# Optimization experiments

Hardware: AMD Instinct MI355X
Metric: run time of the kernel (lower is better)

The kernel has to match this reference:

```python
import jax, jax.numpy as jnp
import numpy as np

EMBED_DIM = 1024
NUM_HEADS = 16
HEAD_DIM = EMBED_DIM // NUM_HEADS


def setup_inputs() -> dict:
    key = jax.random.key(0)
    ks = jax.random.split(key, 9)
    B, S, D = 4, 2048, EMBED_DIM
    s = 1.0 / np.sqrt(D)
    inp = {
        "x": jax.random.normal(ks[0], (B, S, D), dtype=jnp.float32),
        "Wq": jax.random.uniform(ks[1], (D, D), jnp.float32, -s, s),
        "bq": jax.random.uniform(ks[2], (D,), jnp.float32, -s, s),
        "Wk": jax.random.uniform(ks[3], (D, D), jnp.float32, -s, s),
        "bk": jax.random.uniform(ks[4], (D,), jnp.float32, -s, s),
        "Wv": jax.random.uniform(ks[5], (D, D), jnp.float32, -s, s),
        "bv": jax.random.uniform(ks[6], (D,), jnp.float32, -s, s),
        "Wo": jax.random.uniform(ks[7], (D, D), jnp.float32, -s, s),
        "bo": jax.random.uniform(ks[8], (D,), jnp.float32, -s, s),
    }
    return inp


def reference(x, Wq, bq, Wk, bk, Wv, bv, Wo, bo):
    B, S, D = x.shape
    H, Hd = NUM_HEADS, HEAD_DIM
    scale = 1.0 / jnp.sqrt(jnp.asarray(Hd, x.dtype))

    def split_heads(t):  # (B,S,D) -> (B,H,S,Hd)
        return t.reshape(B, S, H, Hd).transpose(0, 2, 1, 3)

    q = split_heads(x @ Wq + bq)
    k = split_heads(x @ Wk + bk)
    v = split_heads(x @ Wv + bv)

    scores = jnp.einsum("bhqd,bhkd->bhqk", q, k) * scale
    attn = jax.nn.softmax(scores, axis=-1)  # dropout is identity in eval mode
    out = jnp.einsum("bhqk,bhkd->bhqd", attn, v)
    out = out.transpose(0, 2, 1, 3).reshape(B, S, D)
    return out @ Wo + bo
```

## Files before the change

### kernel.cpp

```cpp
#include <hip/hip_runtime.h>
#include <cstdint>

typedef unsigned short u16;
typedef uint32_t u32;
typedef float f32x4 __attribute__((ext_vector_type(4)));
typedef short s16x8 __attribute__((ext_vector_type(8)));
typedef u16 u16x4 __attribute__((ext_vector_type(4)));
typedef u32 u32x2 __attribute__((ext_vector_type(2)));
typedef u32 u32x4 __attribute__((ext_vector_type(4)));

__device__ __forceinline__ u16 f2bf(float f) {
  u32 u = __builtin_bit_cast(u32, f);
  u += 0x7FFFu + ((u >> 16) & 1u);
  return (u16)(u >> 16);
}

__device__ __forceinline__ u32 pack2bf_trunc(float lo, float hi) {
  return __builtin_amdgcn_perm(__builtin_bit_cast(u32, hi),
                               __builtin_bit_cast(u32, lo), 0x07060302u);
}

template <typename T>
__device__ __forceinline__ T ldv(const void* p) {
  T v;
  __builtin_memcpy(&v, __builtin_assume_aligned(p, 16), sizeof(T));
  return v;
}

__device__ __forceinline__ void gload_lds16(const void* g, void* l) {
  __builtin_amdgcn_global_load_lds((const __attribute__((address_space(1))) void*)g,
                                   (__attribute__((address_space(3))) void*)l, 16, 0, 0);
}

__global__ __launch_bounds__(256) void cvt_x_k(const float* __restrict__ in,
                                               u16* __restrict__ out) {
  const int i = (blockIdx.x * 256 + threadIdx.x) * 4;
  float4 v = *(const float4*)(in + i);
  u16x4 o;
  o.x = f2bf(v.x); o.y = f2bf(v.y); o.z = f2bf(v.z); o.w = f2bf(v.w);
  *(u16x4*)(out + i) = o;
}

__global__ __launch_bounds__(256) void prep_w_k(const float* __restrict__ Wq,
                                                const float* __restrict__ Wk,
                                                const float* __restrict__ Wv,
                                                const float* __restrict__ Wo,
                                                u16* __restrict__ out) {
  __shared__ u16 t[64][72];
  const float* W = (blockIdx.z == 0) ? Wq : (blockIdx.z == 1) ? Wk
                  : (blockIdx.z == 2) ? Wv : Wo;
  u16* O = out + (size_t)blockIdx.z * 1024 * 1024;
  const int n0 = blockIdx.x * 64, k0 = blockIdx.y * 64;
  const int tid = threadIdx.x;
#pragma unroll
  for (int i = 0; i < 16; ++i) {
    int e = i * 256 + tid;
    int r = e >> 6, c = e & 63;
    t[r][c] = f2bf(W[(size_t)(k0 + r) * 1024 + n0 + c]);
  }
  __syncthreads();
#pragma unroll
  for (int i = 0; i < 16; ++i) {
    int e = i * 256 + tid;
    int rr = e >> 6, cc = e & 63;
    O[(size_t)(n0 + rr) * 1024 + k0 + cc] = t[cc][rr];
  }
}

__global__ __launch_bounds__(256) void gemm_qkv_k(const u16* __restrict__ A,
                                                  const u16* __restrict__ Wt,
                                                  const float* __restrict__ bq,
                                                  const float* __restrict__ bk,
                                                  const float* __restrict__ bv,
                                                  u16* __restrict__ Qh,
                                                  u16* __restrict__ Kh,
                                                  u16* __restrict__ Vt,
                                                  float qscale) {
  constexpr int K = 1024;
  __shared__ __attribute__((aligned(16))) u16 As[2][128][64];
  __shared__ __attribute__((aligned(16))) u16 Bs[2][128][64];
  const int tid = threadIdx.x;
  const int l = tid & 63, w = tid >> 6;
  const int lr = l & 15, lg = l >> 4;
  const int m0 = blockIdx.x * 128;
  const int ng = blockIdx.y * 128;
  const int seg = ng >> 10;
  const int n0 = ng & 1023;
  const u16* Bt = Wt + ((size_t)seg << 20);
  const int wr = (w >> 1) * 64, wc = (w & 1) * 64;
  const int rA = tid >> 3;
  const int cA = (tid & 7) * 8;

  f32x4 acc[4][4] = {};

#define GSTAGE(buf, kt)                                                         \
  do {                                                                          \
    _Pragma("unroll")                                                           \
    for (int i = 0; i < 4; ++i) {                                               \
      gload_lds16(A + (size_t)(m0 + i * 32 + rA) * K + (kt) + cA,               \
                  &As[buf][0][0] + (size_t)(i * 256 + w * 64) * 8);             \
      gload_lds16(Bt + (size_t)(n0 + i * 32 + rA) * K + (kt) + cA,              \
                  &Bs[buf][0][0] + (size_t)(i * 256 + w * 64) * 8);             \
    }                                                                           \
  } while (0)

  GSTAGE(0, 0);
  for (int ki = 0; ki < 16; ++ki) {
    const int cur = ki & 1;
    if (ki < 15) {
      GSTAGE(cur ^ 1, (ki + 1) * 64);
      asm volatile("s_waitcnt vmcnt(8)" ::: "memory");
    } else {
      asm volatile("s_waitcnt vmcnt(0)" ::: "memory");
    }
    __builtin_amdgcn_sched_barrier(0);
    __builtin_amdgcn_s_barrier();
    __builtin_amdgcn_sched_barrier(0);
#pragma unroll
    for (int kk = 0; kk < 2; ++kk) {
      s16x8 a[4], b[4];
#pragma unroll
      for (int mi = 0; mi < 4; ++mi)
        a[mi] = ldv<s16x8>(&As[cur][wr + mi * 16 + lr][kk * 32 + lg * 8]);
#pragma unroll
      for (int ni = 0; ni < 4; ++ni)
        b[ni] = ldv<s16x8>(&Bs[cur][wc + ni * 16 + lr][kk * 32 + lg * 8]);
#pragma unroll
      for (int mi = 0; mi < 4; ++mi)
#pragma unroll
        for (int ni = 0; ni < 4; ++ni)
          acc[mi][ni] = __builtin_amdgcn_mfma_f32_16x16x32_bf16(a[mi], b[ni], acc[mi][ni], 0, 0, 0);
    }
    __builtin_amdgcn_sched_barrier(0);
    __builtin_amdgcn_s_barrier();
  }
#undef GSTAGE

  const float* bias = (seg == 0) ? bq : (seg == 1) ? bk : bv;
  const float scale = (seg == 0) ? qscale : 1.0f;
  u16* outp = (seg == 0) ? Qh : (seg == 1) ? Kh : Vt;

  u16* Cb = &As[0][0][0];
  const int bb = m0 >> 11;
  const int sbase = m0 & 2047;

#pragma unroll
  for (int p = 0; p < 2; ++p) {
    __syncthreads();
    if ((wc >> 6) == p) {
#pragma unroll
      for (int ni = 0; ni < 4; ++ni) {
        const int c = ni * 16 + lr;
        const float bvv = bias[n0 + p * 64 + c];
#pragma unroll
        for (int mi = 0; mi < 4; ++mi) {
#pragma unroll
          for (int r = 0; r < 4; ++r) {
            const int row = wr + mi * 16 + lg * 4 + r;
            Cb[row * 64 + ((((c >> 3) ^ (row & 7)) << 3) | (c & 7))] =
                f2bf((acc[mi][ni][r] + bvv) * scale);
          }
        }
      }
    }
    __syncthreads();
    const int h = (n0 + p * 64) >> 6;
    if (seg <= 1) {
      const int row = tid >> 1;
      const int s = sbase + row;
#pragma unroll
      for (int j = 0; j < 4; ++j) {
        const int c = (tid & 1) * 32 + j * 8;
        s16x8 v = ldv<s16x8>(&Cb[row * 64 + (((c >> 3) ^ (row & 7)) << 3)]);
        const int chunk = (seg == 0) ? (c >> 3) : (((c >> 3) ^ (s & 7)) & 7);
        *(s16x8*)(outp + ((size_t)((bb << 4) + h) * 2048 + s) * 64 + (chunk << 3)) = v;
      }
    } else {
      const int hd = tid & 63;
#pragma unroll
      for (int j = 0; j < 4; ++j) {
        const int s0 = ((tid >> 6) * 4 + j) * 8;
        u16 vals[8];
#pragma unroll
        for (int i = 0; i < 8; ++i) {
          const int row = s0 + i;
          vals[i] = Cb[row * 64 + ((((hd >> 3) ^ (row & 7)) << 3) | (hd & 7))];
        }
        const int sl = sbase + s0;
        const int swz = (((sl >> 3) & 7) ^ (hd & 7)) & 7;
        *(s16x8*)(outp + ((size_t)((bb << 4) + h) * 64 + hd) * 2048 +
                  ((sl & ~63) | (swz << 3))) = *(s16x8*)vals;
      }
    }
  }
}

__global__ __launch_bounds__(256) void gemm_o_k(const u16* __restrict__ A,
                                                const u16* __restrict__ Bt,
                                                const float* __restrict__ bias,
                                                float* __restrict__ outp) {
  constexpr int K = 1024;
  __shared__ __attribute__((aligned(16))) u16 As[2][128][64];
  __shared__ __attribute__((aligned(16))) u16 Bs[2][128][64];
  const int tid = threadIdx.x;
  const int l = tid & 63, w = tid >> 6;
  const int lr = l & 15, lg = l >> 4;
  const int m0 = blockIdx.x * 128, n0 = blockIdx.y * 128;
  const int wr = (w >> 1) * 64, wc = (w & 1) * 64;
  const int rA = tid >> 3;
  const int cA = (tid & 7) * 8;

  f32x4 acc[4][4] = {};

#define GSTAGE(buf, kt)                                                         \
  do {                                                                          \
    _Pragma("unroll")                                                           \
    for (int i = 0; i < 4; ++i) {                                               \
      gload_lds16(A + (size_t)(m0 + i * 32 + rA) * K + (kt) + cA,               \
                  &As[buf][0][0] + (size_t)(i * 256 + w * 64) * 8);             \
      gload_lds16(Bt + (size_t)(n0 + i * 32 + rA) * K + (kt) + cA,              \
                  &Bs[buf][0][0] + (size_t)(i * 256 + w * 64) * 8);             \
    }                                                                           \
  } while (0)

  GSTAGE(0, 0);
  for (int ki = 0; ki < 16; ++ki) {
    const int cur = ki & 1;
    if (ki < 15) {
      GSTAGE(cur ^ 1, (ki + 1) * 64);
      asm volatile("s_waitcnt vmcnt(8)" ::: "memory");
    } else {
      asm volatile("s_waitcnt vmcnt(0)" ::: "memory");
    }
    __builtin_amdgcn_sched_barrier(0);
    __builtin_amdgcn_s_barrier();
    __builtin_amdgcn_sched_barrier(0);
#pragma unroll
    for (int kk = 0; kk < 2; ++kk) {
      s16x8 a[4], b[4];
#pragma unroll
      for (int mi = 0; mi < 4; ++mi)
        a[mi] = ldv<s16x8>(&As[cur][wr + mi * 16 + lr][kk * 32 + lg * 8]);
#pragma unroll
      for (int ni = 0; ni < 4; ++ni)
        b[ni] = ldv<s16x8>(&Bs[cur][wc + ni * 16 + lr][kk * 32 + lg * 8]);
#pragma unroll
      for (int mi = 0; mi < 4; ++mi)
#pragma unroll
        for (int ni = 0; ni < 4; ++ni)
          acc[mi][ni] = __builtin_amdgcn_mfma_f32_16x16x32_bf16(a[mi], b[ni], acc[mi][ni], 0, 0, 0);
    }
    __builtin_amdgcn_sched_barrier(0);
    __builtin_amdgcn_s_barrier();
  }
#undef GSTAGE

#pragma unroll
  for (int ni = 0; ni < 4; ++ni) {
    const int col = n0 + wc + ni * 16 + lr;
    const float bv = bias[col];
#pragma unroll
    for (int mi = 0; mi < 4; ++mi)
#pragma unroll
      for (int r = 0; r < 4; ++r) {
        const int rowm = m0 + wr + mi * 16 + lg * 4 + r;
        outp[(size_t)rowm * 1024 + col] = acc[mi][ni][r] + bv;
      }
  }
}

__global__ __launch_bounds__(256, 4) void attn_k(const u16* __restrict__ Qh,
                                                 const u16* __restrict__ Kg,
                                                 const u16* __restrict__ Vg,
                                                 u16* __restrict__ Oattn) {
  __shared__ __attribute__((aligned(16))) u16 Kbuf[2][4096];
  __shared__ __attribute__((aligned(16))) u16 Vbuf[2][4096];
  __shared__ __attribute__((aligned(16))) u16 P_lds[4][16][64];
  const int tid = threadIdx.x, l = tid & 63, w = tid >> 6;
  const int lr = l & 15, lg = l >> 4;
  const int bh = blockIdx.y;
  const int q0 = blockIdx.x * 128 + w * 32;
  const u16* Q = Qh + (size_t)bh * (2048 * 64);
  const u16* K = Kg + (size_t)bh * (2048 * 64);
  const u16* V = Vg + (size_t)bh * (64 * 2048);

  s16x8 qf[2][2];
#pragma unroll
  for (int f = 0; f < 2; ++f)
#pragma unroll
    for (int kk = 0; kk < 2; ++kk)
      qf[f][kk] = ldv<s16x8>(Q + (size_t)(q0 + f * 16 + lr) * 64 + kk * 32 + lg * 8);

  const u32 one2 = 0x3F803F80u;
  const s16x8 onesv = __builtin_bit_cast(s16x8, (u32x4){one2, one2, one2, one2});

  f32x4 acc[2][4] = {};
  f32x4 lsum[2] = {};

#define STAGE(buf, kv0)                                                                 \
  do {                                                                                  \
    gload_lds16(K + (size_t)(kv0) * 64 + (size_t)tid * 8, &Kbuf[buf][w * 512]);         \
    gload_lds16(K + (size_t)(kv0) * 64 + 2048 + (size_t)tid * 8,                        \
                &Kbuf[buf][2048 + w * 512]);                                            \
    gload_lds16(V + (size_t)(tid >> 3) * 2048 + (kv0) + (tid & 7) * 8,                  \
                &Vbuf[buf][w * 512]);                                                   \
    gload_lds16(V + (size_t)((tid >> 3) + 32) * 2048 + (kv0) + (tid & 7) * 8,           \
                &Vbuf[buf][2048 + w * 512]);                                            \
  } while (0)

  STAGE(0, 0);

  for (int t = 0; t < 32; ++t) {
    const int cur = t & 1;
    if (t < 31) {
      STAGE(cur ^ 1, (t + 1) * 64);
      asm volatile("s_waitcnt vmcnt(4)" ::: "memory");
    } else {
      asm volatile("s_waitcnt vmcnt(0)" ::: "memory");
    }
    __builtin_amdgcn_sched_barrier(0);
    __builtin_amdgcn_s_barrier();
    __builtin_amdgcn_sched_barrier(0);

    f32x4 s[2][4] = {};
    __builtin_amdgcn_s_setprio(1);
#pragma unroll
    for (int tt = 0; tt < 4; ++tt) {
      s16x8 k0 = ldv<s16x8>(&Kbuf[cur][(tt * 16 + lr) * 64 + ((lg ^ (lr & 7)) << 3)]);
      s16x8 k1 = ldv<s16x8>(&Kbuf[cur][(tt * 16 + lr) * 64 + (((4 + lg) ^ (lr & 7)) << 3)]);
#pragma unroll
      for (int f = 0; f < 2; ++f) {
        s[f][tt] = __builtin_amdgcn_mfma_f32_16x16x32_bf16(k0, qf[f][0], s[f][tt], 0, 0, 0);
        s[f][tt] = __builtin_amdgcn_mfma_f32_16x16x32_bf16(k1, qf[f][1], s[f][tt], 0, 0, 0);
      }
    }
    __builtin_amdgcn_s_setprio(0);

    s16x8 pf[2][2];
#pragma unroll
    for (int f = 0; f < 2; ++f) {
#pragma unroll
      for (int tt = 0; tt < 4; ++tt)
#pragma unroll
        for (int r = 0; r < 4; ++r)
          s[f][tt][r] = __builtin_amdgcn_exp2f(s[f][tt][r]);
#pragma unroll
      for (int tt = 0; tt < 4; ++tt) {
        u32x2 pw;
        pw.x = pack2bf_trunc(s[f][tt][0], s[f][tt][1]);
        pw.y = pack2bf_trunc(s[f][tt][2], s[f][tt][3]);
        const int off = (((tt * 2 + (lg >> 1)) ^ (lr & 7)) << 3) + ((lg & 1) << 2);
        *(u32x2*)&P_lds[w][lr][off] = pw;
      }
#pragma unroll
      for (int kvc = 0; kvc < 2; ++kvc)
        pf[f][kvc] = ldv<s16x8>(&P_lds[w][lr][((kvc * 4 + lg) ^ (lr & 7)) << 3]);
      lsum[f] = __builtin_amdgcn_mfma_f32_16x16x32_bf16(pf[f][0], onesv, lsum[f], 0, 0, 0);
      lsum[f] = __builtin_amdgcn_mfma_f32_16x16x32_bf16(pf[f][1], onesv, lsum[f], 0, 0, 0);
    }

    __builtin_amdgcn_s_setprio(1);
#pragma unroll
    for (int dt = 0; dt < 4; ++dt) {
      s16x8 v0 = ldv<s16x8>(&Vbuf[cur][(dt * 16 + lr) * 64 + ((lg ^ (lr & 7)) << 3)]);
      s16x8 v1 = ldv<s16x8>(&Vbuf[cur][(dt * 16 + lr) * 64 + (((4 + lg) ^ (lr & 7)) << 3)]);
#pragma unroll
      for (int f = 0; f < 2; ++f) {
        acc[f][dt] = __builtin_amdgcn_mfma_f32_16x16x32_bf16(pf[f][0], v0, acc[f][dt], 0, 0, 0);
        acc[f][dt] = __builtin_amdgcn_mfma_f32_16x16x32_bf16(pf[f][1], v1, acc[f][dt], 0, 0, 0);
      }
    }
    __builtin_amdgcn_s_setprio(0);
    __builtin_amdgcn_sched_barrier(0);
    __builtin_amdgcn_s_barrier();
  }
#undef STAGE

  const int b = bh >> 4, h = bh & 15;
#pragma unroll
  for (int f = 0; f < 2; ++f) {
    float li[4];
#pragma unroll
    for (int r = 0; r < 4; ++r) li[r] = __builtin_amdgcn_rcpf(lsum[f][r]);
#pragma unroll
    for (int dt = 0; dt < 4; ++dt)
#pragma unroll
      for (int r = 0; r < 4; ++r) {
        const int q = q0 + f * 16 + lg * 4 + r;
        Oattn[(size_t)((b << 11) + q) * 1024 + (h << 6) + dt * 16 + lr] =
            f2bf(acc[f][dt][r] * li[r]);
      }
  }
}

extern "C" void kernel_launch(void* const* d_in, const int* in_sizes, int n_in,
                              void* d_out, int out_size, void* d_ws, size_t ws_size,
                              hipStream_t stream) {
  const float* x  = (const float*)d_in[0];
  const float* Wq = (const float*)d_in[1];
  const float* bq = (const float*)d_in[2];
  const float* Wk = (const float*)d_in[3];
  const float* bk = (const float*)d_in[4];
  const float* Wv = (const float*)d_in[5];
  const float* bv = (const float*)d_in[6];
  const float* Wo = (const float*)d_in[7];
  const float* bo = (const float*)d_in[8];

  char* ws = (char*)d_ws;
  const size_t MB = 1u << 20;
  u16* xb = (u16*)(ws);
  u16* wt = (u16*)(ws + 16 * MB);
  u16* Qh = (u16*)(ws + 24 * MB);
  u16* Kh = (u16*)(ws + 40 * MB);
  u16* Vt = (u16*)(ws + 56 * MB);
  u16* attn = xb;

  const float qscale = 0.125f * 1.44269504088896f;

  cvt_x_k<<<dim3(8192), dim3(256), 0, stream>>>(x, xb);
  prep_w_k<<<dim3(16, 16, 4), dim3(256), 0, stream>>>(Wq, Wk, Wv, Wo, wt);
  gemm_qkv_k<<<dim3(64, 24), dim3(256), 0, stream>>>(xb, wt, bq, bk, bv, Qh, Kh, Vt, qscale);
  attn_k<<<dim3(16, 64), dim3(256), 0, stream>>>(Qh, Kh, Vt, attn);
  gemm_o_k<<<dim3(64, 8), dim3(256), 0, stream>>>(attn, wt + 3 * 1048576, bo, (float*)d_out);
}
```

Measured before the change: 212.9 us.

## Enlarge GEMM tiles to 256x128 with 8 warps and swizzle LDS layout

Both the QKV and output-projection GEMMs move from 128x128 tiles with 4 waves to 256x128 tiles with 8 waves (512 threads), halving the grid along M. The B tile is then shared across twice as many rows, cutting global traffic for the weights. LDS is written and read with an XOR column swizzle to avoid bank conflicts on the MFMA operand loads. Risks: fewer blocks, which may underfill the CUs for the output GEMM (256 blocks), and the epilogue indexing has to match the new warp layout.

```diff
diff --git a/kernel.cpp b/kernel.cpp
--- a/kernel.cpp
+++ b/kernel.cpp
@@ -67,41 +67,42 @@
   }
 }
 
-__global__ __launch_bounds__(256) void gemm_qkv_k(const u16* __restrict__ A,
-                                                  const u16* __restrict__ Wt,
-                                                  const float* __restrict__ bq,
-                                                  const float* __restrict__ bk,
-                                                  const float* __restrict__ bv,
-                                                  u16* __restrict__ Qh,
-                                                  u16* __restrict__ Kh,
-                                                  u16* __restrict__ Vt,
-                                                  float qscale) {
+__global__ __launch_bounds__(512, 2) void gemm_qkv_k(const u16* __restrict__ A,
+                                                     const u16* __restrict__ Wt,
+                                                     const float* __restrict__ bq,
+                                                     const float* __restrict__ bk,
+                                                     const float* __restrict__ bv,
+                                                     u16* __restrict__ Qh,
+                                                     u16* __restrict__ Kh,
+                                                     u16* __restrict__ Vt,
+                                                     float qscale) {
   constexpr int K = 1024;
-  __shared__ __attribute__((aligned(16))) u16 As[2][128][64];
+  __shared__ __attribute__((aligned(16))) u16 As[2][256][64];
   __shared__ __attribute__((aligned(16))) u16 Bs[2][128][64];
   const int tid = threadIdx.x;
   const int l = tid & 63, w = tid >> 6;
   const int lr = l & 15, lg = l >> 4;
-  const int m0 = blockIdx.x * 128;
+  const int m0 = blockIdx.x * 256;
   const int ng = blockIdx.y * 128;
   const int seg = ng >> 10;
   const int n0 = ng & 1023;
   const u16* Bt = Wt + ((size_t)seg << 20);
   const int wr = (w >> 1) * 64, wc = (w & 1) * 64;
-  const int rA = tid >> 3;
-  const int cA = (tid & 7) * 8;
+  const int rT = tid >> 3;
+  const int cSw = (((tid & 7) ^ ((tid >> 3) & 7)) << 3);
 
   f32x4 acc[4][4] = {};
 
 #define GSTAGE(buf, kt)                                                         \
   do {                                                                          \
     _Pragma("unroll")                                                           \
-    for (int i = 0; i < 4; ++i) {                                               \
-      gload_lds16(A + (size_t)(m0 + i * 32 + rA) * K + (kt) + cA,               \
-                  &As[buf][0][0] + (size_t)(i * 256 + w * 64) * 8);             \
-      gload_lds16(Bt + (size_t)(n0 + i * 32 + rA) * K + (kt) + cA,              \
-                  &Bs[buf][0][0] + (size_t)(i * 256 + w * 64) * 8);             \
-    }                                                                           \
+    for (int i = 0; i < 4; ++i)                                                 \
+      gload_lds16(A + (size_t)(m0 + i * 64 + rT) * K + (kt) + cSw,              \
+                  &As[buf][i * 64][0] + (size_t)w * 512);                       \
+    _Pragma("unroll")                                                           \
+    for (int i = 0; i < 2; ++i)                                                 \
+      gload_lds16(Bt + (size_t)(n0 + i * 64 + rT) * K + (kt) + cSw,             \
+                  &Bs[buf][i * 64][0] + (size_t)w * 512);                       \
   } while (0)
 
   GSTAGE(0, 0);
@@ -109,7 +110,7 @@
     const int cur = ki & 1;
     if (ki < 15) {
       GSTAGE(cur ^ 1, (ki + 1) * 64);
-      asm volatile("s_waitcnt vmcnt(8)" ::: "memory");
+      asm volatile("s_waitcnt vmcnt(6)" ::: "memory");
     } else {
       asm volatile("s_waitcnt vmcnt(0)" ::: "memory");
     }
@@ -121,10 +122,10 @@
       s16x8 a[4], b[4];
 #pragma unroll
       for (int mi = 0; mi < 4; ++mi)
-        a[mi] = ldv<s16x8>(&As[cur][wr + mi * 16 + lr][kk * 32 + lg * 8]);
+        a[mi] = ldv<s16x8>(&As[cur][wr + mi * 16 + lr][((kk * 4 + lg) ^ (lr & 7)) << 3]);
 #pragma unroll
       for (int ni = 0; ni < 4; ++ni)
-        b[ni] = ldv<s16x8>(&Bs[cur][wc + ni * 16 + lr][kk * 32 + lg * 8]);
+        b[ni] = ldv<s16x8>(&Bs[cur][wc + ni * 16 + lr][((kk * 4 + lg) ^ (lr & 7)) << 3]);
 #pragma unroll
       for (int mi = 0; mi < 4; ++mi)
 #pragma unroll
@@ -179,7 +180,7 @@
       const int hd = tid & 63;
 #pragma unroll
       for (int j = 0; j < 4; ++j) {
-        const int s0 = ((tid >> 6) * 4 + j) * 8;
+        const int s0 = (tid >> 6) * 32 + j * 8;
         u16 vals[8];
 #pragma unroll
         for (int i = 0; i < 8; ++i) {
@@ -195,32 +196,33 @@
   }
 }
 
-__global__ __launch_bounds__(256) void gemm_o_k(const u16* __restrict__ A,
-                                                const u16* __restrict__ Bt,
-                                                const float* __restrict__ bias,
-                                                float* __restrict__ outp) {
+__global__ __launch_bounds__(512, 2) void gemm_o_k(const u16* __restrict__ A,
+                                                   const u16* __restrict__ Bt,
+                                                   const float* __restrict__ bias,
+                                                   float* __restrict__ outp) {
   constexpr int K = 1024;
-  __shared__ __attribute__((aligned(16))) u16 As[2][128][64];
+  __shared__ __attribute__((aligned(16))) u16 As[2][256][64];
   __shared__ __attribute__((aligned(16))) u16 Bs[2][128][64];
   const int tid = threadIdx.x;
   const int l = tid & 63, w = tid >> 6;
   const int lr = l & 15, lg = l >> 4;
-  const int m0 = blockIdx.x * 128, n0 = blockIdx.y * 128;
+  const int m0 = blockIdx.x * 256, n0 = blockIdx.y * 128;
   const int wr = (w >> 1) * 64, wc = (w & 1) * 64;
-  const int rA = tid >> 3;
-  const int cA = (tid & 7) * 8;
+  const int rT = tid >> 3;
+  const int cSw = (((tid & 7) ^ ((tid >> 3) & 7)) << 3);
 
   f32x4 acc[4][4] = {};
 
 #define GSTAGE(buf, kt)                                                         \
   do {                                                                          \
     _Pragma("unroll")                                                           \
-    for (int i = 0; i < 4; ++i) {                                               \
-      gload_lds16(A + (size_t)(m0 + i * 32 + rA) * K + (kt) + cA,               \
-                  &As[buf][0][0] + (size_t)(i * 256 + w * 64) * 8);             \
-      gload_lds16(Bt + (size_t)(n0 + i * 32 + rA) * K + (kt) + cA,              \
-                  &Bs[buf][0][0] + (size_t)(i * 256 + w * 64) * 8);             \
-    }                                                                           \
+    for (int i = 0; i < 4; ++i)                                                 \
+      gload_lds16(A + (size_t)(m0 + i * 64 + rT) * K + (kt) + cSw,              \
+                  &As[buf][i * 64][0] + (size_t)w * 512);                       \
+    _Pragma("unroll")                                                           \
+    for (int i = 0; i < 2; ++i)                                                 \
+      gload_lds16(Bt + (size_t)(n0 + i * 64 + rT) * K + (kt) + cSw,             \
+                  &Bs[buf][i * 64][0] + (size_t)w * 512);                       \
   } while (0)
 
   GSTAGE(0, 0);
@@ -228,7 +230,7 @@
     const int cur = ki & 1;
     if (ki < 15) {
       GSTAGE(cur ^ 1, (ki + 1) * 64);
-      asm volatile("s_waitcnt vmcnt(8)" ::: "memory");
+      asm volatile("s_waitcnt vmcnt(6)" ::: "memory");
     } else {
       asm volatile("s_waitcnt vmcnt(0)" ::: "memory");
     }
@@ -240,10 +242,10 @@
       s16x8 a[4], b[4];
 #pragma unroll
       for (int mi = 0; mi < 4; ++mi)
-        a[mi] = ldv<s16x8>(&As[cur][wr + mi * 16 + lr][kk * 32 + lg * 8]);
+        a[mi] = ldv<s16x8>(&As[cur][wr + mi * 16 + lr][((kk * 4 + lg) ^ (lr & 7)) << 3]);
 #pragma unroll
       for (int ni = 0; ni < 4; ++ni)
-        b[ni] = ldv<s16x8>(&Bs[cur][wc + ni * 16 + lr][kk * 32 + lg * 8]);
+        b[ni] = ldv<s16x8>(&Bs[cur][wc + ni * 16 + lr][((kk * 4 + lg) ^ (lr & 7)) << 3]);
 #pragma unroll
       for (int mi = 0; mi < 4; ++mi)
 #pragma unroll
@@ -419,7 +421,7 @@
 
   cvt_x_k<<<dim3(8192), dim3(256), 0, stream>>>(x, xb);
   prep_w_k<<<dim3(16, 16, 4), dim3(256), 0, stream>>>(Wq, Wk, Wv, Wo, wt);
-  gemm_qkv_k<<<dim3(64, 24), dim3(256), 0, stream>>>(xb, wt, bq, bk, bv, Qh, Kh, Vt, qscale);
+  gemm_qkv_k<<<dim3(32, 24), dim3(512), 0, stream>>>(xb, wt, bq, bk, bv, Qh, Kh, Vt, qscale);
   attn_k<<<dim3(16, 64), dim3(256), 0, stream>>>(Qh, Kh, Vt, attn);
-  gemm_o_k<<<dim3(64, 8), dim3(256), 0, stream>>>(attn, wt + 3 * 1048576, bo, (float*)d_out);
-}
+  gemm_o_k<<<dim3(32, 8), dim3(512), 0, stream>>>(attn, wt + 3 * 1048576, bo, (float*)d_out);
+}
```

Result: no change. 209.7 us (-1.5%).
